# Performance work log

Hardware: AMD Instinct MI355X
Metric: run time of the kernel (lower is better)

## Reference

```python
import jax, jax.numpy as jnp
import numpy as np

B, L, SRC_DIM = 64, 384, 512
HID, EMB = 512, 256
NUM_CLASSES = 250
NUM_STEPS = 127  # batch_max_length(128) - 1


def setup_inputs() -> dict:
    key = jax.random.key(0)
    ks = jax.random.split(key, 13)
    s = 0.05
    return {
        "src": jax.random.normal(ks[0], (B, L, SRC_DIM), jnp.float32),
        "text": jax.random.randint(ks[1], (B, NUM_STEPS), 0, NUM_CLASSES + 1),
        "emb_table": jax.random.normal(ks[2], (NUM_CLASSES + 1, EMB), jnp.float32) * s,
        "Wi2h": jax.random.normal(ks[3], (HID, SRC_DIM), jnp.float32) * s,
        "Wh2h": jax.random.normal(ks[4], (HID, HID), jnp.float32) * s,
        "bh2h": jax.random.normal(ks[5], (HID,), jnp.float32) * s,
        "wscore": jax.random.normal(ks[6], (HID,), jnp.float32) * s,
        "W_ih": jax.random.normal(ks[7], (4 * HID, SRC_DIM + EMB), jnp.float32) * s,
        "b_ih": jax.random.normal(ks[8], (4 * HID,), jnp.float32) * s,
        "W_hh": jax.random.normal(ks[9], (4 * HID, HID), jnp.float32) * s,
        "b_hh": jax.random.normal(ks[10], (4 * HID,), jnp.float32) * s,
        "Wgen": jax.random.normal(ks[11], (NUM_CLASSES, HID), jnp.float32) * s,
        "bgen": jax.random.normal(ks[12], (NUM_CLASSES,), jnp.float32) * s,
    }


def reference(src, text, emb_table, Wi2h, Wh2h, bh2h, wscore,
              W_ih, b_ih, W_hh, b_hh, Wgen, bgen):
    """ASTERDecoder teacher-forced forward (num_layers=1).
    src: [B, L, C]; text: [B, T] int tokens. Returns probs [B, T, num_classes].
    """
    b = src.shape[0]
    H = Wh2h.shape[0]
    # i2h(src) is constant across decode steps -> hoist out of the loop.
    src_feat = jnp.einsum('blc,hc->blh', src, Wi2h)          # [B, L, H]
    emb_seq = emb_table[text]                                # [B, T, E]

    def step(carry, emb_t):
        h, c = carry                                         # [B, H] each
        proj = h @ Wh2h.T + bh2h                             # h2h(prev_hidden)
        # Bahdanau score + softmax over L, then context via weighted sum.
        logit = jnp.tanh(src_feat + proj[:, None, :]) @ wscore   # [B, L]
        alpha = jax.nn.softmax(logit, axis=1)
        context = jnp.einsum('bl,blc->bc', alpha, src)       # [B, C]
        x = jnp.concatenate([context, emb_t], axis=1)        # [B, C+E]
        # LSTMCell gates (PyTorch order: i, f, g, o)
        gates = x @ W_ih.T + b_ih + h @ W_hh.T + b_hh        # [B, 4H]
        i, f, g, o = jnp.split(gates, 4, axis=1)
        i, f, o = jax.nn.sigmoid(i), jax.nn.sigmoid(f), jax.nn.sigmoid(o)
        g = jnp.tanh(g)
        c_new = f * c + i * g
        h_new = o * jnp.tanh(c_new)
        return (h_new, c_new), h_new

    init = (jnp.zeros((b, H), src.dtype), jnp.zeros((b, H), src.dtype))
    _, hs = jax.lax.scan(step, init, jnp.swapaxes(emb_seq, 0, 1))  # hs: [T, B, H]
    output_hiddens = jnp.swapaxes(hs, 0, 1)                  # [B, T, H]
    probs = jnp.einsum('bth,nh->btn', output_hiddens, Wgen) + bgen
    return probs
```

## Files before the change

### kernel.cpp

```cpp
#include <hip/hip_runtime.h>

typedef unsigned short u16;
typedef unsigned int   u32;
typedef _Float16 f16;
typedef f16   f16x2 __attribute__((ext_vector_type(2)));
typedef f16   f16x8 __attribute__((ext_vector_type(8)));
typedef float f32x4 __attribute__((ext_vector_type(4)));
typedef u32   u32x4 __attribute__((ext_vector_type(4)));

#define B_  64
#define L_  384
#define CS  512
#define H_  512
#define E_  256
#define NC  250
#define T_  127
#define MSHIFT 20.0f

__device__ __forceinline__ float h2f(u16 u){ f16 h; __builtin_memcpy(&h,&u,2); return (float)h; }
__device__ __forceinline__ u16  f2h(float f){ f16 h=(f16)f; u16 u; __builtin_memcpy(&u,&h,2); return u; }
__device__ __forceinline__ float wredsum(float v){
#pragma unroll
  for (int o=32;o>0;o>>=1) v += __shfl_down(v, o, 64);
  return v;
}
__device__ __forceinline__ float tanh_f(float x){
  x = fminf(fmaxf(x, -15.f), 15.f);
  float e = __expf(2.f*x);
  return (e-1.f)/(e+1.f);
}
__device__ __forceinline__ float sigm_f(float x){
  x = fminf(fmaxf(x, -30.f), 30.f);
  return 1.f/(1.f+__expf(-x));
}
__device__ __forceinline__ float dot2f(u32 a, u32 b, float c){
  f16x2 x, y; __builtin_memcpy(&x,&a,4); __builtin_memcpy(&y,&b,4);
#if __has_builtin(__builtin_amdgcn_fdot2)
  return __builtin_amdgcn_fdot2(x, y, c, false);
#else
  return c + (float)x[0]*(float)y[0] + (float)x[1]*(float)y[1];
#endif
}

__global__ __launch_bounds__(256) void k_cvt(const float* __restrict__ in, f16* __restrict__ o, int n){
  int i = blockIdx.x*256 + threadIdx.x;
  if (i < n) o[i] = (f16)in[i];
}

__global__ __launch_bounds__(256) void k_packwhq(const float* __restrict__ Wh, u32* __restrict__ Wq){
  int i = blockIdx.x*256 + threadIdx.x;
  if (i < 64*512*4){
    int kq = i >> 11, n = (i >> 2) & 511, e = i & 3;
    int k = kq*8 + e*2;
    u32 lo = f2h(Wh[(size_t)n*512 + k]);
    u32 hi = f2h(Wh[(size_t)n*512 + k + 1]);
    Wq[i] = lo | (hi<<16);
  }
}

__global__ __launch_bounds__(256) void k_packwcp(const float* __restrict__ Wih, f16* __restrict__ Wcp){
  int i = blockIdx.x*256 + threadIdx.x;
  if (i < 2048*512){
    int pc = i >> 9, k = i & 511;
    int r = (pc&3)*512 + (pc>>2);
    Wcp[i] = (f16)Wih[(size_t)r*768 + k];
  }
}

__global__ __launch_bounds__(256) void k_packwgp2(const float* __restrict__ Wih,
    const float* __restrict__ Whh, const float* __restrict__ bih, const float* __restrict__ bhh,
    f16* __restrict__ WgP, float* __restrict__ bias_g){
  int i = blockIdx.x*256 + threadIdx.x;
  if (i < 2048*768){
    int pc = i / 768, k = i - pc*768;
    int r = (pc&3)*512 + (pc>>2);
    float v = (k < 256) ? Wih[(size_t)r*768 + 512 + k] : Whh[(size_t)r*512 + (k-256)];
    WgP[i] = (f16)v;
    if (k == 0) bias_g[pc] = bih[r] + bhh[r];
  }
}

__global__ __launch_bounds__(256) void k_emb(const int* __restrict__ text,
    const float* __restrict__ embt, f16* __restrict__ embseq){
  int i = blockIdx.x*256 + threadIdx.x;
  if (i < B_*T_*E_){
    int bt = i >> 8, col = i & 255;
    int tok = text[bt];
    embseq[i] = (f16)embt[(size_t)tok*E_ + col];
  }
}

__global__ __launch_bounds__(256) void k_sf_mfma(
    const float* __restrict__ A, const f16* __restrict__ Wn, u16* __restrict__ Cd, int N)
{
  int w = threadIdx.x >> 6, lane = threadIdx.x & 63;
  int quad = lane >> 4, l16 = lane & 15;
  int m0 = blockIdx.x * 64;
  int nb = blockIdx.y * 256 + w * 64;
  const float* ap0 = A  + (size_t)(m0 + l16)*512 + quad*8;
  const f16*   bp0 = Wn + (size_t)(nb + l16)*512 + quad*8;
  f32x4 acc[4][4] = {};
  for (int k0=0; k0<512; k0+=32){
    f16x8 bfr[4];
#pragma unroll
    for (int nt=0; nt<4; nt++)
      bfr[nt] = *(const f16x8*)(bp0 + (size_t)nt*16*512 + k0);
#pragma unroll
    for (int f=0; f<4; f++){
      const float* ap = ap0 + (size_t)f*16*512 + k0;
      float4 a0 = *(const float4*)ap;
      float4 a1 = *(const float4*)(ap+4);
      f16x8 afr = { (f16)a0.x,(f16)a0.y,(f16)a0.z,(f16)a0.w,
                    (f16)a1.x,(f16)a1.y,(f16)a1.z,(f16)a1.w };
#pragma unroll
      for (int nt=0; nt<4; nt++)
        acc[f][nt] = __builtin_amdgcn_mfma_f32_16x16x32_f16(afr, bfr[nt], acc[f][nt], 0,0,0);
    }
  }
#pragma unroll
  for (int f=0; f<4; f++)
#pragma unroll
    for (int nt=0; nt<4; nt++)
#pragma unroll
      for (int r=0; r<4; r++){
        int m = m0 + f*16 + quad*4 + r;
        int n = nb + nt*16 + l16;
        Cd[(size_t)m*N + n] = f2h(acc[f][nt][r]);
      }
}

__global__ __launch_bounds__(256) void k_probs_mfma(
    const u16* __restrict__ A, const f16* __restrict__ Wn,
    const float* __restrict__ bias, float* __restrict__ Cd)
{
  int w = threadIdx.x >> 6, lane = threadIdx.x & 63;
  int quad = lane >> 4, l16 = lane & 15;
  int m0 = blockIdx.x * 64;
  int nb = w * 64;
  const f16* ap0 = (const f16*)A + (size_t)(m0 + l16)*512 + quad*8;
  const f16* bp0 = Wn + (size_t)(nb + l16)*512 + quad*8;
  f32x4 acc[4][4] = {};
  for (int k0=0; k0<512; k0+=32){
    f16x8 bfr[4];
#pragma unroll
    for (int nt=0; nt<4; nt++)
      bfr[nt] = *(const f16x8*)(bp0 + (size_t)nt*16*512 + k0);
#pragma unroll
    for (int f=0; f<4; f++){
      f16x8 afr = *(const f16x8*)(ap0 + (size_t)f*16*512 + k0);
#pragma unroll
      for (int nt=0; nt<4; nt++)
        acc[f][nt] = __builtin_amdgcn_mfma_f32_16x16x32_f16(afr, bfr[nt], acc[f][nt], 0,0,0);
    }
  }
#pragma unroll
  for (int f=0; f<4; f++)
#pragma unroll
    for (int nt=0; nt<4; nt++)
#pragma unroll
      for (int r=0; r<4; r++){
        int m = m0 + f*16 + quad*4 + r;
        int n = nb + nt*16 + l16;
        if (n < NC) Cd[(size_t)m*NC + n] = acc[f][nt][r] + bias[n];
      }
}

__global__ __launch_bounds__(512) void k_stepA(
    const u32* __restrict__ WhQ, const u16* __restrict__ sf,
    const f16* __restrict__ src16, const f16* __restrict__ hbuf,
    const float* __restrict__ bh2h, const float* __restrict__ wsc,
    const f16* __restrict__ WgP, const float* __restrict__ bias_g,
    const f16* __restrict__ embseq,
    float* __restrict__ ctxp, float* __restrict__ denp,
    float* __restrict__ gpart, int t)
{
  const int tid = threadIdx.x;
  const int wid = tid >> 6, lane = tid & 63;

  if (blockIdx.x < 256){
    const int b = blockIdx.x >> 2;
    const int q = blockIdx.x & 3;
    __shared__ __align__(16) u32 sh_h2[256];
    __shared__ float sh_proj[512];
    __shared__ float sh_e[96];
    __shared__ float sh_cp[8][512];

    if (tid < 256) sh_h2[tid] = ((const u32*)(hbuf + (size_t)b*512))[tid];
    __syncthreads();
    {
      const u32* wp = WhQ + ((size_t)tid << 2);
      const u32x4* hp = (const u32x4*)sh_h2;
      float a0=0.f, a1=0.f, a2=0.f, a3=0.f;
#pragma unroll 8
      for (int kq=0; kq<64; kq++){
        u32x4 wq = *(const u32x4*)(wp + ((size_t)kq << 11));
        u32x4 hq = hp[kq];
        a0 = dot2f(wq.x, hq.x, a0);
        a1 = dot2f(wq.y, hq.y, a1);
        a2 = dot2f(wq.z, hq.z, a2);
        a3 = dot2f(wq.w, hq.w, a3);
      }
      sh_proj[tid] = (a0+a1) + (a2+a3) + bh2h[tid];
    }
    __syncthreads();
    {
      float pv[8], wv[8];
#pragma unroll
      for (int j=0;j<8;j++){ pv[j]=sh_proj[lane*8+j]; wv[j]=wsc[lane*8+j]; }
      const int l0 = q*96 + wid*12;
      const f16* sp0 = (const f16*)sf + (((size_t)(b*L_ + l0)) << 9) + lane*8;
#pragma unroll 4
      for (int i=0;i<12;i++){
        f16x8 s = *(const f16x8*)(sp0 + ((size_t)i << 9));
        float v;
        v  = tanh_f((float)s[0]+pv[0])*wv[0];
        v += tanh_f((float)s[1]+pv[1])*wv[1];
        v += tanh_f((float)s[2]+pv[2])*wv[2];
        v += tanh_f((float)s[3]+pv[3])*wv[3];
        v += tanh_f((float)s[4]+pv[4])*wv[4];
        v += tanh_f((float)s[5]+pv[5])*wv[5];
        v += tanh_f((float)s[6]+pv[6])*wv[6];
        v += tanh_f((float)s[7]+pv[7])*wv[7];
        v = wredsum(v);
        if (lane == 0) sh_e[wid*12 + i] = __expf(v - MSHIFT);
      }
    }
    __syncthreads();
    if (wid == 0){
      float v = sh_e[lane] + (lane < 32 ? sh_e[64+lane] : 0.f);
      v = wredsum(v);
      if (lane == 0) denp[q*64 + b] = v;
    }
    {
      float acc[8] = {0.f,0.f,0.f,0.f,0.f,0.f,0.f,0.f};
      const f16* sp0 = src16 + (((size_t)(b*L_ + q*96 + wid*12)) << 9) + lane*8;
      const float* alp = sh_e + wid*12;
#pragma unroll 4
      for (int i=0;i<12;i++){
        f16x8 v = *(const f16x8*)(sp0 + ((size_t)i << 9));
        float al = alp[i];
#pragma unroll
        for (int e=0;e<8;e++) acc[e] += al*(float)v[e];
      }
#pragma unroll
      for (int e=0;e<8;e++) sh_cp[wid][lane*8+e] = acc[e];
    }
    __syncthreads();
    if (tid < 256){
      int c0 = tid*2;
      float v0 = (((sh_cp[0][c0]+sh_cp[1][c0])+(sh_cp[2][c0]+sh_cp[3][c0]))
                + ((sh_cp[4][c0]+sh_cp[5][c0])+(sh_cp[6][c0]+sh_cp[7][c0])));
      int c1 = c0+1;
      float v1 = (((sh_cp[0][c1]+sh_cp[1][c1])+(sh_cp[2][c1]+sh_cp[3][c1]))
                + ((sh_cp[4][c1]+sh_cp[5][c1])+(sh_cp[6][c1]+sh_cp[7][c1])));
      float2 o; o.x = v0; o.y = v1;
      *(float2*)(ctxp + (((size_t)(q*64 + b)) << 9) + c0) = o;
    }
  } else {
    const int j = blockIdx.x - 256;
    const int quad = lane >> 4, l16 = lane & 15;
    const int n = j*128 + wid*16 + l16;
    const f16* bp = WgP + (size_t)n*768 + quad*8;
    f32x4 acc[4] = {};
    for (int k0=0; k0<256; k0+=32){
      f16x8 bfr = *(const f16x8*)(bp + k0);
#pragma unroll
      for (int f=0; f<4; f++){
        int br = f*16 + l16;
        f16x8 afr = *(const f16x8*)(embseq + (((size_t)(br*T_ + t)) << 8) + quad*8 + k0);
        acc[f] = __builtin_amdgcn_mfma_f32_16x16x32_f16(afr, bfr, acc[f], 0,0,0);
      }
    }
    for (int k0=0; k0<512; k0+=32){
      f16x8 bfr = *(const f16x8*)(bp + 256 + k0);
#pragma unroll
      for (int f=0; f<4; f++){
        int br = f*16 + l16;
        f16x8 afr = *(const f16x8*)(hbuf + (size_t)br*512 + quad*8 + k0);
        acc[f] = __builtin_amdgcn_mfma_f32_16x16x32_f16(afr, bfr, acc[f], 0,0,0);
      }
    }
    float bias = bias_g[n];
#pragma unroll
    for (int f=0; f<4; f++)
#pragma unroll
      for (int r=0; r<4; r++){
        int b2 = f*16 + quad*4 + r;
        gpart[((size_t)b2 << 11) + n] = acc[f][r] + bias;
      }
  }
}

__global__ __launch_bounds__(256) void k_stepB(
    const float* __restrict__ ctxp, const float* __restrict__ denp,
    const float* __restrict__ gpart, const f16* __restrict__ Wcp,
    float* __restrict__ cbuf, f16* __restrict__ hbuf, u16* __restrict__ hs, int t)
{
  __shared__ f16   sh_ctx[64][520];
  __shared__ float gbuf[64][17];
  __shared__ float sh_inv[64];
  const int tid = threadIdx.x;
  const int wid = tid >> 6, lane = tid & 63;
  const int quad = lane >> 4, l16 = lane & 15;
  const int j = blockIdx.x;

  if (tid < 64)
    sh_inv[tid] = 1.f/(((denp[tid] + denp[64+tid]) + (denp[128+tid] + denp[192+tid])));
  __syncthreads();

#pragma unroll 4
  for (int i=0;i<32;i++){
    int flat = tid + i*256;
    int b = flat >> 7, c4 = flat & 127;
    const float* base = ctxp + ((size_t)b << 9) + (c4 << 2);
    float4 v0 = *(const float4*)(base);
    float4 v1 = *(const float4*)(base + (64<<9));
    float4 v2 = *(const float4*)(base + (128<<9));
    float4 v3 = *(const float4*)(base + (192<<9));
    float inv = sh_inv[b];
    int c = c4*4;
    sh_ctx[b][c+0] = (f16)(((v0.x+v1.x)+(v2.x+v3.x))*inv);
    sh_ctx[b][c+1] = (f16)(((v0.y+v1.y)+(v2.y+v3.y))*inv);
    sh_ctx[b][c+2] = (f16)(((v0.z+v1.z)+(v2.z+v3.z))*inv);
    sh_ctx[b][c+3] = (f16)(((v0.w+v1.w)+(v2.w+v3.w))*inv);
  }
  __syncthreads();

  {
    const f16* bp = Wcp + (size_t)(j*16 + l16)*512 + quad*8;
    const f16* ap = &sh_ctx[wid*16 + l16][quad*8];
    f32x4 acc = {};
#pragma unroll
    for (int k0=0; k0<512; k0+=32)
      acc = __builtin_amdgcn_mfma_f32_16x16x32_f16(*(const f16x8*)(ap + k0),
                                                   *(const f16x8*)(bp + k0), acc, 0,0,0);
#pragma unroll
    for (int r=0;r<4;r++) gbuf[wid*16 + quad*4 + r][l16] = acc[r];
  }
  __syncthreads();

  {
    const int b2 = tid >> 2, hl = tid & 3;
    const int hd = j*4 + hl;
    float4 gp = *(const float4*)(gpart + ((size_t)b2 << 11) + (size_t)hd*4);
    float gi = gbuf[b2][hl*4+0] + gp.x;
    float gf = gbuf[b2][hl*4+1] + gp.y;
    float gg = gbuf[b2][hl*4+2] + gp.z;
    float go = gbuf[b2][hl*4+3] + gp.w;
    float fi=sigm_f(gi), ff=sigm_f(gf), fg=tanh_f(gg), fo=sigm_f(go);
    size_t ci = ((size_t)b2 << 9) + hd;
    float cn = ff*cbuf[ci] + fi*fg;
    float hn = fo*tanh_f(cn);
    cbuf[ci] = cn;
    hbuf[((size_t)b2 << 9) + hd] = (f16)hn;
    hs[((size_t)(b2*T_ + t)) * 512 + hd] = f2h(hn);
  }
}

extern "C" void kernel_launch(void* const* d_in, const int* in_sizes, int n_in,
                              void* d_out, int out_size, void* d_ws, size_t ws_size,
                              hipStream_t stream)
{
  const float* src   = (const float*)d_in[0];
  const int*   text  = (const int*)d_in[1];
  const float* embt  = (const float*)d_in[2];
  const float* Wi2h  = (const float*)d_in[3];
  const float* Wh2h  = (const float*)d_in[4];
  const float* bh2h  = (const float*)d_in[5];
  const float* wsc   = (const float*)d_in[6];
  const float* W_ih  = (const float*)d_in[7];
  const float* b_ih  = (const float*)d_in[8];
  const float* W_hh  = (const float*)d_in[9];
  const float* b_hh  = (const float*)d_in[10];
  const float* Wgen  = (const float*)d_in[11];
  const float* bgen  = (const float*)d_in[12];
  float* out = (float*)d_out;

  char* p = (char*)d_ws;
  u16*   sfw    = (u16*)p;    p += (size_t)B_*L_*H_*2;
  u16*   hsw    = (u16*)p;    p += (size_t)B_*T_*H_*2;
  f16*   src16  = (f16*)p;    p += (size_t)B_*L_*CS*2;
  u32*   WhQ    = (u32*)p;    p += (size_t)64*512*4*4;
  f16*   Wi2h16 = (f16*)p;    p += (size_t)H_*CS*2;
  f16*   Wcp    = (f16*)p;    p += (size_t)2048*512*2;
  f16*   WgP    = (f16*)p;    p += (size_t)2048*768*2;
  f16*   Wgen16 = (f16*)p;    p += (size_t)256*512*2;
  f16*   embseq = (f16*)p;    p += (size_t)B_*T_*E_*2;
  f16*   hbuf   = (f16*)p;    p += (size_t)B_*H_*2;
  float* ctxp   = (float*)p;  p += (size_t)4*B_*512*4;
  float* denp   = (float*)p;  p += (size_t)256*4;
  float* gpart  = (float*)p;  p += (size_t)B_*2048*4;
  float* cbuf   = (float*)p;  p += (size_t)B_*H_*4;
  float* bias_g = (float*)p;  p += (size_t)2048*4;

  hipMemsetAsync(hbuf,   0, (size_t)B_*H_*2, stream);
  hipMemsetAsync(cbuf,   0, (size_t)B_*H_*4, stream);
  hipMemsetAsync(Wgen16, 0, (size_t)256*512*2, stream);

  k_cvt     <<<(H_*CS+255)/256,    256, 0, stream>>>(Wi2h, Wi2h16, H_*CS);
  k_cvt     <<<(B_*L_*CS+255)/256, 256, 0, stream>>>(src, src16, B_*L_*CS);
  k_cvt     <<<(NC*512+255)/256,   256, 0, stream>>>(Wgen, (f16*)Wgen16, NC*512);
  k_packwhq <<<(64*512*4+255)/256, 256, 0, stream>>>(Wh2h, WhQ);
  k_packwcp <<<(2048*512+255)/256, 256, 0, stream>>>(W_ih, Wcp);
  k_packwgp2<<<(2048*768+255)/256, 256, 0, stream>>>(W_ih, W_hh, b_ih, b_hh, WgP, bias_g);
  k_emb     <<<(B_*T_*E_+255)/256, 256, 0, stream>>>(text, embt, embseq);

  k_sf_mfma<<<dim3(384,2), 256, 0, stream>>>(src, Wi2h16, sfw, 512);

  for (int t=0; t<T_; t++){
    k_stepA<<<272, 512, 0, stream>>>(WhQ, sfw, src16, hbuf, bh2h, wsc,
                                     WgP, bias_g, embseq, ctxp, denp, gpart, t);
    k_stepB<<<128, 256, 0, stream>>>(ctxp, denp, gpart, Wcp, cbuf, hbuf, hsw, t);
  }

  k_probs_mfma<<<127, 256, 0, stream>>>(hsw, Wgen16, bgen, out);
}
```

Before: 6.085 ms.

## Consolidate stepB into 32 larger blocks to cut redundant context reduction

The per-step LSTM finalize kernel now runs 32 blocks of 512 threads instead of 128 blocks of 256. Each block covers 16 hidden units (64 gate rows), so the duplicated per-block reduction of the context partials into shared memory happens 4x less often. Each wave reuses one weight fragment across two batch tiles. Context stores are packed into 4-wide shared writes. The trade-off is far fewer blocks on a GPU with many CUs, which lowers parallelism for the MFMA and gate work.

```diff
diff --git a/kernel.cpp b/kernel.cpp
--- a/kernel.cpp
+++ b/kernel.cpp
@@ -291,26 +291,26 @@
   }
 }
 
-__global__ __launch_bounds__(256) void k_stepB(
+__global__ __launch_bounds__(512) void k_stepB(
     const float* __restrict__ ctxp, const float* __restrict__ denp,
     const float* __restrict__ gpart, const f16* __restrict__ Wcp,
     float* __restrict__ cbuf, f16* __restrict__ hbuf, u16* __restrict__ hs, int t)
 {
   __shared__ f16   sh_ctx[64][520];
-  __shared__ float gbuf[64][17];
+  __shared__ float sh_g[4][64][17];
   __shared__ float sh_inv[64];
   const int tid = threadIdx.x;
   const int wid = tid >> 6, lane = tid & 63;
   const int quad = lane >> 4, l16 = lane & 15;
-  const int j = blockIdx.x;
+  const int j2 = blockIdx.x;
 
   if (tid < 64)
     sh_inv[tid] = 1.f/(((denp[tid] + denp[64+tid]) + (denp[128+tid] + denp[192+tid])));
   __syncthreads();
 
 #pragma unroll 4
-  for (int i=0;i<32;i++){
-    int flat = tid + i*256;
+  for (int i=0;i<16;i++){
+    int flat = tid + i*512;
     int b = flat >> 7, c4 = flat & 127;
     const float* base = ctxp + ((size_t)b << 9) + (c4 << 2);
     float4 v0 = *(const float4*)(base);
@@ -318,35 +318,47 @@
     float4 v2 = *(const float4*)(base + (128<<9));
     float4 v3 = *(const float4*)(base + (192<<9));
     float inv = sh_inv[b];
-    int c = c4*4;
-    sh_ctx[b][c+0] = (f16)(((v0.x+v1.x)+(v2.x+v3.x))*inv);
-    sh_ctx[b][c+1] = (f16)(((v0.y+v1.y)+(v2.y+v3.y))*inv);
-    sh_ctx[b][c+2] = (f16)(((v0.z+v1.z)+(v2.z+v3.z))*inv);
-    sh_ctx[b][c+3] = (f16)(((v0.w+v1.w)+(v2.w+v3.w))*inv);
+    ushort4 o;
+    o.x = f2h(((v0.x+v1.x)+(v2.x+v3.x))*inv);
+    o.y = f2h(((v0.y+v1.y)+(v2.y+v3.y))*inv);
+    o.z = f2h(((v0.z+v1.z)+(v2.z+v3.z))*inv);
+    o.w = f2h(((v0.w+v1.w)+(v2.w+v3.w))*inv);
+    *(ushort4*)&sh_ctx[b][c4*4] = o;
   }
   __syncthreads();
 
   {
-    const f16* bp = Wcp + (size_t)(j*16 + l16)*512 + quad*8;
-    const f16* ap = &sh_ctx[wid*16 + l16][quad*8];
-    f32x4 acc = {};
-#pragma unroll
-    for (int k0=0; k0<512; k0+=32)
-      acc = __builtin_amdgcn_mfma_f32_16x16x32_f16(*(const f16x8*)(ap + k0),
-                                                   *(const f16x8*)(bp + k0), acc, 0,0,0);
-#pragma unroll
-    for (int r=0;r<4;r++) gbuf[wid*16 + quad*4 + r][l16] = acc[r];
+    const int wrow = wid & 3, half = wid >> 2;
+    const f16* bp = Wcp + (size_t)(j2*64 + wrow*16 + l16)*512 + quad*8;
+    f32x4 acc[2] = {};
+    for (int k0=0; k0<512; k0+=32){
+      f16x8 bfr = *(const f16x8*)(bp + k0);
+#pragma unroll
+      for (int ff=0; ff<2; ff++){
+        int f = half*2 + ff;
+        f16x8 afr = *(const f16x8*)&sh_ctx[f*16 + l16][k0 + quad*8];
+        acc[ff] = __builtin_amdgcn_mfma_f32_16x16x32_f16(afr, bfr, acc[ff], 0,0,0);
+      }
+    }
+#pragma unroll
+    for (int ff=0; ff<2; ff++)
+#pragma unroll
+      for (int r=0; r<4; r++)
+        sh_g[wrow][(half*2+ff)*16 + quad*4 + r][l16] = acc[ff][r];
   }
   __syncthreads();
 
-  {
-    const int b2 = tid >> 2, hl = tid & 3;
-    const int hd = j*4 + hl;
+#pragma unroll
+  for (int it=0; it<2; ++it){
+    int flat = tid + it*512;
+    int b2 = flat >> 4, hl = flat & 15;
+    int w = hl >> 2, rb = (hl & 3) * 4;
+    int hd = j2*16 + hl;
     float4 gp = *(const float4*)(gpart + ((size_t)b2 << 11) + (size_t)hd*4);
-    float gi = gbuf[b2][hl*4+0] + gp.x;
-    float gf = gbuf[b2][hl*4+1] + gp.y;
-    float gg = gbuf[b2][hl*4+2] + gp.z;
-    float go = gbuf[b2][hl*4+3] + gp.w;
+    float gi = sh_g[w][b2][rb+0] + gp.x;
+    float gf = sh_g[w][b2][rb+1] + gp.y;
+    float gg = sh_g[w][b2][rb+2] + gp.z;
+    float go = sh_g[w][b2][rb+3] + gp.w;
     float fi=sigm_f(gi), ff=sigm_f(gf), fg=tanh_f(gg), fo=sigm_f(go);
     size_t ci = ((size_t)b2 << 9) + hd;
     float cn = ff*cbuf[ci] + fi*fg;
@@ -410,7 +422,7 @@
   for (int t=0; t<T_; t++){
     k_stepA<<<272, 512, 0, stream>>>(WhQ, sfw, src16, hbuf, bh2h, wsc,
                                      WgP, bias_g, embseq, ctxp, denp, gpart, t);
-    k_stepB<<<128, 256, 0, stream>>>(ctxp, denp, gpart, Wcp, cbuf, hbuf, hsw, t);
+    k_stepB<<<32, 512, 0, stream>>>(ctxp, denp, gpart, Wcp, cbuf, hbuf, hsw, t);
   }
 
   k_probs_mfma<<<127, 256, 0, stream>>>(hsw, Wgen16, bgen, out);
```

Result: slower. 6.271 ms (+3.1%).
